# Optimization experiments

Hardware: AMD Instinct MI355X
Metric: run time of the kernel (lower is better)

## Reference

```python
import jax, jax.numpy as jnp
import numpy as np

H, E, D, S, B = 16, 1024, 64, 2048, 4  # heads, emb, head_size, seq_len, batch

def setup_inputs() -> dict:
    key = jax.random.key(0)
    ks = jax.random.split(key, 9)
    sc_e = 1.0 / np.sqrt(E)
    sc_hd = 1.0 / np.sqrt(H * D)
    return {
        "x":  jax.random.normal(ks[0], (B, S, E), dtype=jnp.float32),
        # per-head q/k/v projection weights, stacked: [H, E, D]
        "Wq": jax.random.uniform(ks[1], (H, E, D), jnp.float32, -sc_e, sc_e),
        "Wk": jax.random.uniform(ks[2], (H, E, D), jnp.float32, -sc_e, sc_e),
        "Wv": jax.random.uniform(ks[3], (H, E, D), jnp.float32, -sc_e, sc_e),
        "bq": jax.random.uniform(ks[4], (H, D), jnp.float32, -sc_e, sc_e),
        "bk": jax.random.uniform(ks[5], (H, D), jnp.float32, -sc_e, sc_e),
        "bv": jax.random.uniform(ks[6], (H, D), jnp.float32, -sc_e, sc_e),
        # output projection: Linear(H*D -> E)
        "Wo": jax.random.uniform(ks[7], (H * D, E), jnp.float32, -sc_hd, sc_hd),
        "bo": jax.random.uniform(ks[8], (E,), jnp.float32, -sc_hd, sc_hd),
    }

def reference(x, Wq, Wk, Wv, bq, bk, bv, Wo, bo):
    b, s, e = x.shape
    # batched per-head projections: [B, H, S, D]
    q = jnp.einsum("bse,hed->bhsd", x, Wq) + bq[None, :, None, :]
    k = jnp.einsum("bse,hed->bhsd", x, Wk) + bk[None, :, None, :]
    v = jnp.einsum("bse,hed->bhsd", x, Wv) + bv[None, :, None, :]
    scale = 1.0 / jnp.sqrt(jnp.asarray(q.shape[-1], q.dtype))
    scores = jnp.einsum("bhqd,bhkd->bhqk", q, k) * scale  # [B,H,S,S]
    causal = jnp.tril(jnp.ones((s, s), dtype=bool))
    scores = jnp.where(causal[None, None], scores, jnp.asarray(-jnp.inf, scores.dtype))
    attn = jax.nn.softmax(scores, axis=-1)
    heads = jnp.einsum("bhqk,bhkd->bhqd", attn, v)  # [B,H,S,D]
    concat = heads.transpose(0, 2, 1, 3).reshape(b, s, -1)  # [B,S,H*D]
    return concat @ Wo + bo  # dropout is identity at inference
```

## Files before the change

### kernel.cpp

```cpp
#include <hip/hip_runtime.h>
#include <hip/hip_bf16.h>

#define H_ 16
#define E_ 1024
#define D_ 64
#define S_ 2048
#define B_ 4
#define M_ (B_ * S_)

typedef __bf16 bf16_t;
typedef __bf16 bf16x8 __attribute__((ext_vector_type(8)));
typedef __bf16 bf16x4 __attribute__((ext_vector_type(4)));
typedef float f32x4 __attribute__((ext_vector_type(4)));

typedef __attribute__((address_space(1))) unsigned int gu32;
typedef __attribute__((address_space(3))) unsigned int lu32;

__device__ __forceinline__ f32x4 mfma16(bf16x8 a, bf16x8 b, f32x4 c) {
  return __builtin_amdgcn_mfma_f32_16x16x32_bf16(a, b, c, 0, 0, 0);
}
__device__ __forceinline__ void gl2lds16(const bf16_t* g, bf16_t* l) {
  __builtin_amdgcn_global_load_lds((const gu32*)g, (lu32*)l, 16, 0, 0);
}

#define BAR() asm volatile("s_barrier" ::: "memory")

__device__ __forceinline__ int detect_f32(const unsigned short* __restrict__ xu) {
  int lane = threadIdx.x & 63;
  int cnt = 0;
  for (int i = 0; i < 4; ++i) {
    unsigned short v = xu[(lane * 4 + i) * 2];
    cnt += __popcll(__ballot(((v >> 7) & 0xFF) >= 0xC0));
  }
  return cnt > 16;
}

__global__ __launch_bounds__(256) void convert_x(
    const void* __restrict__ src, bf16_t* __restrict__ dst,
    int* __restrict__ flag, long n) {
  const int f32 = detect_f32((const unsigned short*)src);
  if (blockIdx.x == 0 && threadIdx.x == 0) { flag[0] = f32; flag[1] = 0; }
  long i = ((long)blockIdx.x * 256 + threadIdx.x) * 8;
  if (i >= n) return;
  bf16x8 v;
  if (f32) {
    const float* s = (const float*)src;
    for (int j = 0; j < 8; ++j) v[j] = (bf16_t)s[i + j];
  } else {
    v = *(const bf16x8*)((const bf16_t*)src + i);
  }
  *(bf16x8*)(dst + i) = v;
}

__global__ __launch_bounds__(256) void transpose_k(
    const void* __restrict__ src_, bf16_t* __restrict__ dst,
    const int* __restrict__ flag, int K, int N, long sStride, long dStride) {
  __shared__ __align__(16) bf16_t tile[64][72];
  const int f32 = *flag;
  dst += (long)blockIdx.z * dStride;
  const int tk = blockIdx.x * 64, tn = blockIdx.y * 64;
  const int t = threadIdx.x;
  for (int i = 0; i < 2; ++i) {
    int c = t + i * 256;
    int r = c >> 3, col = (c & 7) * 8;
    if (f32) {
      const float* s = (const float*)src_ + (long)blockIdx.z * sStride;
      const float* p = &s[(long)(tk + r) * N + tn + col];
      for (int j = 0; j < 8; ++j) tile[r][col + j] = (bf16_t)p[j];
    } else {
      const bf16_t* s = (const bf16_t*)src_ + (long)blockIdx.z * sStride;
      *(bf16x8*)&tile[r][col] = *(const bf16x8*)&s[(long)(tk + r) * N + tn + col];
    }
  }
  __syncthreads();
  for (int i = 0; i < 2; ++i) {
    int c = t + i * 256;
    int r = c >> 3, col = (c & 7) * 8;
    bf16x8 v;
    for (int j = 0; j < 8; ++j) v[j] = tile[col + j][r];
    *(bf16x8*)&dst[(long)(tn + r) * K + tk + col] = v;
  }
}

__global__ __launch_bounds__(256) void transpose_qkv(
    const void* __restrict__ s0, const void* __restrict__ s1,
    const void* __restrict__ s2,
    bf16_t* __restrict__ d0, bf16_t* __restrict__ d1, bf16_t* __restrict__ d2,
    const int* __restrict__ flag) {
  __shared__ __align__(16) bf16_t tile[64][72];
  const int f32 = *flag;
  const int which = blockIdx.z >> 4, h = blockIdx.z & 15;
  const void* src_ = which == 0 ? s0 : (which == 1 ? s1 : s2);
  bf16_t* dst = (which == 0 ? d0 : (which == 1 ? d1 : d2)) + (long)h * E_ * D_;
  const long sOff = (long)h * E_ * D_;
  const int tk = blockIdx.x * 64;
  const int t = threadIdx.x;
  for (int i = 0; i < 2; ++i) {
    int c = t + i * 256;
    int r = c >> 3, col = (c & 7) * 8;
    if (f32) {
      const float* s = (const float*)src_ + sOff;
      const float* p = &s[(long)(tk + r) * D_ + col];
      for (int j = 0; j < 8; ++j) tile[r][col + j] = (bf16_t)p[j];
    } else {
      const bf16_t* s = (const bf16_t*)src_ + sOff;
      *(bf16x8*)&tile[r][col] = *(const bf16x8*)&s[(long)(tk + r) * D_ + col];
    }
  }
  __syncthreads();
  for (int i = 0; i < 2; ++i) {
    int c = t + i * 256;
    int r = c >> 3, col = (c & 7) * 8;
    bf16x8 v;
    for (int j = 0; j < 8; ++j) v[j] = tile[col + j][r];
    *(bf16x8*)&dst[(long)r * E_ + tk + col] = v;
  }
}

template <int NBF, int KIND>
__global__ __launch_bounds__(512, 2) void gemm8(
    const bf16_t* __restrict__ A, const bf16_t* __restrict__ Bt,
    const void* __restrict__ bias0, const void* __restrict__ bias1,
    const void* __restrict__ bias2,
    bf16_t* __restrict__ Cq, void* __restrict__ Cout,
    const int* __restrict__ flag) {
  __shared__ __align__(16) bf16_t LA[2 * 256 * 64];
  __shared__ __align__(16) bf16_t LB[2 * NBF * 64 * 64];
  const int t = threadIdx.x;
  const int wave = t >> 6, lane = t & 63;
  const int quad = lane >> 4, l16 = lane & 15;
  const int wm = (wave >> 2) * 128;
  const int wn = (wave & 3) * (NBF * 16);
  const int bid = blockIdx.x;
  const int xcd = bid & 7, l = bid >> 3;
  const int m0 = (xcd * 4 + (l & 3)) * 256;
  const int n0 = (l >> 2) * (NBF * 64);

  f32x4 acc[8][NBF] = {};

  const int sr = lane >> 3;
  const int sj = ((lane & 7) ^ sr) << 3;
  auto stA = [&](int u, int tt, int buf) {
    bf16_t* lp = &LA[buf * 16384 + u * 4096 + wave * 512];
    if constexpr (KIND == 0) {
      gl2lds16(&A[(long)(m0 + u * 64 + wave * 8 + sr) * 1024 + tt * 64 + sj], lp);
    } else {
      int m = m0 + u * 64 + wave * 8 + sr;
      int b = m >> 11, s = m & (S_ - 1);
      gl2lds16(&A[(((long)(b * H_ + tt)) * S_ + s) * D_ + sj], lp);
    }
  };
  auto stB = [&](int u, int tt, int buf) {
    bf16_t* lp = &LB[buf * (NBF * 4096) + u * 4096 + wave * 512];
    gl2lds16(&Bt[(long)(n0 + u * 64 + wave * 8 + sr) * 1024 + tt * 64 + sj], lp);
  };
  auto stage = [&](int tt, int buf) {
    stB(0, tt, buf); stB(1, tt, buf);
    if constexpr (NBF == 3) stB(2, tt, buf);
    stA(0, tt, buf); stA(1, tt, buf); stA(2, tt, buf); stA(3, tt, buf);
  };

  auto rdA = [&](int buf, int i, int kk) {
    int R = wm + i * 16 + l16;
    return *(const bf16x8*)&LA[buf * 16384 + R * 64 + (((kk * 4 + quad) ^ (R & 7)) << 3)];
  };
  auto rdB = [&](int buf, int j, int kk) {
    int R = wn + j * 16 + l16;
    return *(const bf16x8*)&LB[buf * (NBF * 4096) + R * 64 + (((kk * 4 + quad) ^ (R & 7)) << 3)];
  };
  auto compute = [&](int buf) {
    bf16x8 a0[8], a1[8], b0[NBF], b1[NBF];
#pragma unroll
    for (int j = 0; j < NBF; ++j) b0[j] = rdB(buf, j, 0);
#pragma unroll
    for (int i = 0; i < 8; ++i) a0[i] = rdA(buf, i, 0);
#pragma unroll
    for (int j = 0; j < NBF; ++j) b1[j] = rdB(buf, j, 1);
#pragma unroll
    for (int i = 0; i < 8; ++i) a1[i] = rdA(buf, i, 1);
    __builtin_amdgcn_s_setprio(1);
#pragma unroll
    for (int i = 0; i < 8; ++i)
#pragma unroll
      for (int j = 0; j < NBF; ++j)
        acc[i][j] = mfma16(b0[j], a0[i], acc[i][j]);
#pragma unroll
    for (int i = 0; i < 8; ++i)
#pragma unroll
      for (int j = 0; j < NBF; ++j)
        acc[i][j] = mfma16(b1[j], a1[i], acc[i][j]);
    __builtin_amdgcn_s_setprio(0);
  };

  stage(0, 0);

#pragma unroll 1
  for (int tt = 0; tt < 14; tt += 2) {
    stage(tt + 1, 1);
    asm volatile("s_waitcnt vmcnt(%0)" :: "n"(NBF + 4) : "memory");
    BAR();
    compute(0);
    BAR();
    stage(tt + 2, 0);
    asm volatile("s_waitcnt vmcnt(%0)" :: "n"(NBF + 4) : "memory");
    BAR();
    compute(1);
    BAR();
  }
  stage(15, 1);
  asm volatile("s_waitcnt vmcnt(%0)" :: "n"(NBF + 4) : "memory");
  BAR();
  compute(0);
  BAR();
  asm volatile("s_waitcnt vmcnt(0)" ::: "memory");
  BAR();
  compute(1);

  const int f32io = flag[0];
  if constexpr (KIND == 0) {
#pragma unroll
    for (int i = 0; i < 8; ++i) {
      const int m = m0 + wm + i * 16 + l16;
      const int b = m >> 11, s = m & (S_ - 1);
#pragma unroll
      for (int j = 0; j < NBF; ++j) {
        const int n = n0 + wn + j * 16 + quad * 4;
        const int which = n >> 10, nin = n & 1023;
        const int h = nin >> 6, d = nin & 63;
        const void* bp = which == 0 ? bias0 : (which == 1 ? bias1 : bias2);
        bf16x4 o;
#pragma unroll
        for (int r = 0; r < 4; ++r) {
          float bv = f32io ? ((const float*)bp)[nin + r]
                           : (float)((const bf16_t*)bp)[nin + r];
          o[r] = (bf16_t)(acc[i][j][r] + bv);
        }
        *(bf16x4*)&Cq[(long)which * (B_ * H_ * S_ * D_) +
                      (((long)(b * H_ + h)) * S_ + s) * D_ + d] = o;
      }
    }
  } else {
#pragma unroll
    for (int i = 0; i < 8; ++i) {
      const long m = m0 + wm + i * 16 + l16;
#pragma unroll
      for (int j = 0; j < NBF; ++j) {
        const int n = n0 + wn + j * 16 + quad * 4;
        if (f32io) {
          f32x4 o;
#pragma unroll
          for (int r = 0; r < 4; ++r)
            o[r] = acc[i][j][r] + ((const float*)bias0)[n + r];
          *(f32x4*)&((float*)Cout)[m * 1024 + n] = o;
        } else {
          bf16x4 o;
#pragma unroll
          for (int r = 0; r < 4; ++r)
            o[r] = (bf16_t)(acc[i][j][r] + (float)((const bf16_t*)bias0)[n + r]);
          *(bf16x4*)&((bf16_t*)Cout)[m * 1024 + n] = o;
        }
      }
    }
  }
}

__global__ __launch_bounds__(256) void attn_k(
    bf16_t* QO,
    const bf16_t* __restrict__ Kg_,
    const bf16_t* __restrict__ Vtg_) {
  __shared__ __align__(16) bf16_t Ks[64 * 64];
  __shared__ __align__(16) bf16_t Vs[64 * 64];
  __shared__ __align__(16) bf16_t Pq[4][32 * 72];
  const int t = threadIdx.x;
  const int wave = t >> 6, lane = t & 63;
  const int quad = lane >> 4, l16 = lane & 15;
  const int bid = blockIdx.x;
  const int qb = 15 - (bid >> 6);
  const int bh = bid & 63;
  const long base = (long)bh * S_ * D_;
  bf16_t* Qg = QO + base;
  const bf16_t* Kg = Kg_ + base;
  const bf16_t* Vt = Vtg_ + base;
  const int q0 = qb * 128, qrl = wave * 32;
  const int rot = ((lane & 7) - (lane >> 3)) & 7;

  bf16x8 qf[2][2];
  for (int n = 0; n < 2; ++n) {
    long row = q0 + qrl + n * 16 + l16;
    bf16x8 a = *(const bf16x8*)&Qg[row * D_ + quad * 8];
    bf16x8 b = *(const bf16x8*)&Qg[row * D_ + 32 + quad * 8];
    for (int j = 0; j < 8; ++j) {
      a[j] = (bf16_t)((float)a[j] * 0.18033688f);
      b[j] = (bf16_t)((float)b[j] * 0.18033688f);
    }
    qf[n][0] = a; qf[n][1] = b;
  }
  bf16x8 ones;
  for (int j = 0; j < 8; ++j) ones[j] = (bf16_t)1.0f;
  f32x4 o_acc[2][4] = {};
  f32x4 lacc[2] = {};

  const int nkt = 2 * qb + 2;
  for (int kt = 0; kt < nkt; ++kt) {
    __syncthreads();
    for (int i = 0; i < 2; ++i) {
      int c = wave * 2 + i;
      gl2lds16(&Kg[(long)(kt * 64 + c * 8 + (lane >> 3)) * D_ + rot * 8],
               &Ks[c * 512]);
      gl2lds16(&Vt[(long)(c * 8 + (lane >> 3)) * S_ + kt * 64 + rot * 8],
               &Vs[c * 512]);
    }
    __syncthreads();

    if (kt * 64 > q0 + qrl + 31) continue;

    f32x4 sc[2][4];
    for (int mt = 0; mt < 4; ++mt) {
      int krow = mt * 16 + l16;
      bf16x8 kf0 = *(const bf16x8*)&Ks[krow * 64 + (((quad + krow) & 7) << 3)];
      bf16x8 kf1 = *(const bf16x8*)&Ks[krow * 64 + (((quad + 4 + krow) & 7) << 3)];
      for (int n = 0; n < 2; ++n) {
        f32x4 z = {0.f, 0.f, 0.f, 0.f};
        z = mfma16(kf0, qf[n][0], z);
        z = mfma16(kf1, qf[n][1], z);
        sc[n][mt] = z;
      }
    }
    if (kt * 64 + 63 > q0 + qrl) {
      for (int n = 0; n < 2; ++n) {
        int qr = q0 + qrl + n * 16 + l16;
        for (int mt = 0; mt < 4; ++mt)
          for (int r = 0; r < 4; ++r) {
            int kc = kt * 64 + mt * 16 + quad * 4 + r;
            if (kc > qr) sc[n][mt][r] = -1e30f;
          }
      }
    }
    for (int n = 0; n < 2; ++n)
      for (int mt = 0; mt < 4; ++mt) {
        bf16x4 pb;
        for (int r = 0; r < 4; ++r)
          pb[r] = (bf16_t)__builtin_amdgcn_exp2f(sc[n][mt][r]);
        *(bf16x4*)&Pq[wave][(n * 16 + l16) * 72 + mt * 16 + quad * 4] = pb;
      }
    bf16x8 pf[2][2];
    for (int m = 0; m < 2; ++m) {
      pf[m][0] = *(const bf16x8*)&Pq[wave][(m * 16 + l16) * 72 + quad * 8];
      pf[m][1] = *(const bf16x8*)&Pq[wave][(m * 16 + l16) * 72 + 32 + quad * 8];
    }
    for (int m = 0; m < 2; ++m) {
      lacc[m] = mfma16(pf[m][0], ones, lacc[m]);
      lacc[m] = mfma16(pf[m][1], ones, lacc[m]);
    }
    for (int dt = 0; dt < 4; ++dt) {
      int drow = dt * 16 + l16;
      bf16x8 vf0 = *(const bf16x8*)&Vs[drow * 64 + (((quad + drow) & 7) << 3)];
      bf16x8 vf1 = *(const bf16x8*)&Vs[drow * 64 + (((quad + 4 + drow) & 7) << 3)];
      for (int m = 0; m < 2; ++m) {
        o_acc[m][dt] = mfma16(pf[m][0], vf0, o_acc[m][dt]);
        o_acc[m][dt] = mfma16(pf[m][1], vf1, o_acc[m][dt]);
      }
    }
  }
  for (int m = 0; m < 2; ++m)
    for (int r = 0; r < 4; ++r) {
      float inv = 1.0f / lacc[m][r];
      long qg = q0 + qrl + m * 16 + quad * 4 + r;
      for (int dt = 0; dt < 4; ++dt)
        Qg[qg * D_ + dt * 16 + l16] = (bf16_t)(o_acc[m][dt][r] * inv);
    }
}

extern "C" void kernel_launch(void* const* d_in, const int* in_sizes, int n_in,
                              void* d_out, int out_size, void* d_ws, size_t ws_size,
                              hipStream_t stream) {
  (void)in_sizes; (void)n_in; (void)out_size; (void)ws_size;
  const void* x  = d_in[0];
  const void* Wq = d_in[1];
  const void* Wk = d_in[2];
  const void* Wv = d_in[3];
  const void* bq = d_in[4];
  const void* bk = d_in[5];
  const void* bv = d_in[6];
  const void* Wo = d_in[7];
  const void* bo = d_in[8];

  char* base = (char*)d_ws;
  int* flag = (int*)base;
  bf16_t* p = (bf16_t*)(base + 16);
  bf16_t* xb_ = p; p += (size_t)M_ * E_;
  bf16_t* qo_ = p; p += (size_t)B_ * H_ * S_ * D_;
  bf16_t* kb_ = p; p += (size_t)B_ * H_ * S_ * D_;
  bf16_t* vb_ = p; p += (size_t)B_ * H_ * S_ * D_;
  bf16_t* wqt = p; p += (size_t)H_ * D_ * E_;
  bf16_t* wkt = p; p += (size_t)H_ * D_ * E_;
  bf16_t* wvt = p; p += (size_t)H_ * D_ * E_;
  bf16_t* wot = p; p += (size_t)E_ * E_;

  convert_x<<<(M_ * E_) / (256 * 8), 256, 0, stream>>>(x, xb_, flag, (long)M_ * E_);

  transpose_qkv<<<dim3(16, 1, 48), 256, 0, stream>>>(Wq, Wk, Wv, wqt, wkt, wvt, flag);
  transpose_k<<<dim3(16, 16, 1), 256, 0, stream>>>(Wo, wot, flag, E_, E_, 0, 0);

  gemm8<3, 0><<<dim3(512), 512, 0, stream>>>(
      xb_, wqt, bq, bk, bv, qo_, nullptr, flag);

  transpose_k<<<dim3(S_ / 64, 1, B_ * H_), 256, 0, stream>>>(
      vb_, xb_, flag + 1, S_, D_, (long)S_ * D_, (long)S_ * D_);

  attn_k<<<dim3(1024), 256, 0, stream>>>(qo_, kb_, xb_);

  gemm8<2, 1><<<dim3(256), 512, 0, stream>>>(
      qo_, wot, bo, nullptr, nullptr, nullptr, d_out, flag);
}
```

Measured before the change: 278.6 us.

## Split GEMM main loop into four barrier-separated phases with staggered LDS staging

Restructures the projection GEMM main loop from two big compute blocks per double-buffer step into four phases. Each phase loads half of the A fragments (and B fragments every other phase) and then issues its MFMAs. Global-to-LDS staging is split into a main part (B plus A chunks 0 and 2) and a rest part (A chunks 1 and 3). These are issued at different points so that refilling a buffer overlaps with the phases still reading the other rows. This cuts live fragment registers and spreads memory traffic more evenly across compute. In exchange it adds more workgroup barriers per k-step, and its correctness depends on the exact row-to-wave mapping of the partial staging.

```diff
diff --git a/kernel.cpp b/kernel.cpp
--- a/kernel.cpp
+++ b/kernel.cpp
@@ -154,10 +154,13 @@
     bf16_t* lp = &LB[buf * (NBF * 4096) + u * 4096 + wave * 512];
     gl2lds16(&Bt[(long)(n0 + u * 64 + wave * 8 + sr) * 1024 + tt * 64 + sj], lp);
   };
-  auto stage = [&](int tt, int buf) {
+  auto stage_main = [&](int tt, int buf) {
     stB(0, tt, buf); stB(1, tt, buf);
     if constexpr (NBF == 3) stB(2, tt, buf);
-    stA(0, tt, buf); stA(1, tt, buf); stA(2, tt, buf); stA(3, tt, buf);
+    stA(0, tt, buf); stA(2, tt, buf);
+  };
+  auto stage_rest = [&](int tt, int buf) {
+    stA(1, tt, buf); stA(3, tt, buf);
   };
 
   auto rdA = [&](int buf, int i, int kk) {
@@ -168,53 +171,46 @@
     int R = wn + j * 16 + l16;
     return *(const bf16x8*)&LB[buf * (NBF * 4096) + R * 64 + (((kk * 4 + quad) ^ (R & 7)) << 3)];
   };
-  auto compute = [&](int buf) {
-    bf16x8 a0[8], a1[8], b0[NBF], b1[NBF];
-#pragma unroll
-    for (int j = 0; j < NBF; ++j) b0[j] = rdB(buf, j, 0);
-#pragma unroll
-    for (int i = 0; i < 8; ++i) a0[i] = rdA(buf, i, 0);
-#pragma unroll
-    for (int j = 0; j < NBF; ++j) b1[j] = rdB(buf, j, 1);
-#pragma unroll
-    for (int i = 0; i < 8; ++i) a1[i] = rdA(buf, i, 1);
+
+  bf16x8 afr[4], bfr[NBF];
+  auto phase = [&](int buf, int kk, int up, bool rb) {
+#pragma unroll
+    for (int i = 0; i < 4; ++i) afr[i] = rdA(buf, up * 4 + i, kk);
+    if (rb) {
+#pragma unroll
+      for (int j = 0; j < NBF; ++j) bfr[j] = rdB(buf, j, kk);
+    }
+    BAR();
     __builtin_amdgcn_s_setprio(1);
 #pragma unroll
-    for (int i = 0; i < 8; ++i)
+    for (int i = 0; i < 4; ++i)
 #pragma unroll
       for (int j = 0; j < NBF; ++j)
-        acc[i][j] = mfma16(b0[j], a0[i], acc[i][j]);
-#pragma unroll
-    for (int i = 0; i < 8; ++i)
-#pragma unroll
-      for (int j = 0; j < NBF; ++j)
-        acc[i][j] = mfma16(b1[j], a1[i], acc[i][j]);
+        acc[up * 4 + i][j] = mfma16(bfr[j], afr[i], acc[up * 4 + i][j]);
     __builtin_amdgcn_s_setprio(0);
   };
 
-  stage(0, 0);
+  stage_main(0, 0); stage_rest(0, 0);
+  stage_main(1, 1);
+  asm volatile("s_waitcnt vmcnt(%0)" :: "n"(NBF + 2) : "memory");
+  BAR();
 
 #pragma unroll 1
-  for (int tt = 0; tt < 14; tt += 2) {
-    stage(tt + 1, 1);
-    asm volatile("s_waitcnt vmcnt(%0)" :: "n"(NBF + 4) : "memory");
+  for (int T = 0; T < 16; ++T) {
+    const int b = T & 1;
+    if (T < 15) stage_rest(T + 1, b ^ 1);
+    phase(b, 0, 0, true);
     BAR();
-    compute(0);
+    phase(b, 0, 1, false);
     BAR();
-    stage(tt + 2, 0);
-    asm volatile("s_waitcnt vmcnt(%0)" :: "n"(NBF + 4) : "memory");
+    phase(b, 1, 0, true);
     BAR();
-    compute(1);
+    if (T < 14) stage_main(T + 2, b);
+    phase(b, 1, 1, false);
+    if (T < 14) asm volatile("s_waitcnt vmcnt(%0)" :: "n"(NBF + 2) : "memory");
+    else        asm volatile("s_waitcnt vmcnt(0)" ::: "memory");
     BAR();
   }
-  stage(15, 1);
-  asm volatile("s_waitcnt vmcnt(%0)" :: "n"(NBF + 4) : "memory");
-  BAR();
-  compute(0);
-  BAR();
-  asm volatile("s_waitcnt vmcnt(0)" ::: "memory");
-  BAR();
-  compute(1);
 
   const int f32io = flag[0];
   if constexpr (KIND == 0) {
```

New measurement: 313.3 us. 12.5% more time.

## Double-buffer K/V tiles in attention kernel with async prefetch

Applied to the files above, without the earlier changes.

Doubles the LDS K and V buffers. The attention loop now issues the global-to-LDS loads for the next key tile before computing on the current one, using explicit vmcnt waits and barriers so the load latency overlaps with MFMA work. This adds 16KB of LDS per block, which may lower occupancy. It relies on BAR() being defined elsewhere in the file and on the vmcnt count matching the four outstanding loads.

```diff
diff --git a/kernel.cpp b/kernel.cpp
--- a/kernel.cpp
+++ b/kernel.cpp
@@ -268,8 +268,8 @@
     bf16_t* QO,
     const bf16_t* __restrict__ Kg_,
     const bf16_t* __restrict__ Vtg_) {
-  __shared__ __align__(16) bf16_t Ks[64 * 64];
-  __shared__ __align__(16) bf16_t Vs[64 * 64];
+  __shared__ __align__(16) bf16_t Ks[2 * 64 * 64];
+  __shared__ __align__(16) bf16_t Vs[2 * 64 * 64];
   __shared__ __align__(16) bf16_t Pq[4][32 * 72];
   const int t = threadIdx.x;
   const int wave = t >> 6, lane = t & 63;
@@ -284,6 +284,17 @@
   const int q0 = qb * 128, qrl = wave * 32;
   const int rot = ((lane & 7) - (lane >> 3)) & 7;
 
+  auto stageKV = [&](int kt, int buf) {
+    for (int i = 0; i < 2; ++i) {
+      int c = wave * 2 + i;
+      gl2lds16(&Kg[(long)(kt * 64 + c * 8 + (lane >> 3)) * D_ + rot * 8],
+               &Ks[buf * 4096 + c * 512]);
+      gl2lds16(&Vt[(long)(c * 8 + (lane >> 3)) * S_ + kt * 64 + rot * 8],
+               &Vs[buf * 4096 + c * 512]);
+    }
+  };
+  stageKV(0, 0);
+
   bf16x8 qf[2][2];
   for (int n = 0; n < 2; ++n) {
     long row = q0 + qrl + n * 16 + l16;
@@ -301,66 +312,68 @@
   f32x4 lacc[2] = {};
 
   const int nkt = 2 * qb + 2;
+#pragma unroll 1
   for (int kt = 0; kt < nkt; ++kt) {
-    __syncthreads();
-    for (int i = 0; i < 2; ++i) {
-      int c = wave * 2 + i;
-      gl2lds16(&Kg[(long)(kt * 64 + c * 8 + (lane >> 3)) * D_ + rot * 8],
-               &Ks[c * 512]);
-      gl2lds16(&Vt[(long)(c * 8 + (lane >> 3)) * S_ + kt * 64 + rot * 8],
-               &Vs[c * 512]);
-    }
-    __syncthreads();
-
-    if (kt * 64 > q0 + qrl + 31) continue;
-
-    f32x4 sc[2][4];
-    for (int mt = 0; mt < 4; ++mt) {
-      int krow = mt * 16 + l16;
-      bf16x8 kf0 = *(const bf16x8*)&Ks[krow * 64 + (((quad + krow) & 7) << 3)];
-      bf16x8 kf1 = *(const bf16x8*)&Ks[krow * 64 + (((quad + 4 + krow) & 7) << 3)];
-      for (int n = 0; n < 2; ++n) {
-        f32x4 z = {0.f, 0.f, 0.f, 0.f};
-        z = mfma16(kf0, qf[n][0], z);
-        z = mfma16(kf1, qf[n][1], z);
-        sc[n][mt] = z;
-      }
-    }
-    if (kt * 64 + 63 > q0 + qrl) {
-      for (int n = 0; n < 2; ++n) {
-        int qr = q0 + qrl + n * 16 + l16;
-        for (int mt = 0; mt < 4; ++mt)
-          for (int r = 0; r < 4; ++r) {
-            int kc = kt * 64 + mt * 16 + quad * 4 + r;
-            if (kc > qr) sc[n][mt][r] = -1e30f;
-          }
-      }
-    }
-    for (int n = 0; n < 2; ++n)
+    const int buf = kt & 1;
+    const int kb = buf * 4096;
+    if (kt + 1 < nkt) {
+      stageKV(kt + 1, buf ^ 1);
+      asm volatile("s_waitcnt vmcnt(4)" ::: "memory");
+    } else {
+      asm volatile("s_waitcnt vmcnt(0)" ::: "memory");
+    }
+    BAR();
+
+    if (kt * 64 <= q0 + qrl + 31) {
+      f32x4 sc[2][4];
       for (int mt = 0; mt < 4; ++mt) {
-        bf16x4 pb;
-        for (int r = 0; r < 4; ++r)
-          pb[r] = (bf16_t)__builtin_amdgcn_exp2f(sc[n][mt][r]);
-        *(bf16x4*)&Pq[wave][(n * 16 + l16) * 72 + mt * 16 + quad * 4] = pb;
-      }
-    bf16x8 pf[2][2];
-    for (int m = 0; m < 2; ++m) {
-      pf[m][0] = *(const bf16x8*)&Pq[wave][(m * 16 + l16) * 72 + quad * 8];
-      pf[m][1] = *(const bf16x8*)&Pq[wave][(m * 16 + l16) * 72 + 32 + quad * 8];
-    }
-    for (int m = 0; m < 2; ++m) {
-      lacc[m] = mfma16(pf[m][0], ones, lacc[m]);
-      lacc[m] = mfma16(pf[m][1], ones, lacc[m]);
-    }
-    for (int dt = 0; dt < 4; ++dt) {
-      int drow = dt * 16 + l16;
-      bf16x8 vf0 = *(const bf16x8*)&Vs[drow * 64 + (((quad + drow) & 7) << 3)];
-      bf16x8 vf1 = *(const bf16x8*)&Vs[drow * 64 + (((quad + 4 + drow) & 7) << 3)];
+        int krow = mt * 16 + l16;
+        bf16x8 kf0 = *(const bf16x8*)&Ks[kb + krow * 64 + (((quad + krow) & 7) << 3)];
+        bf16x8 kf1 = *(const bf16x8*)&Ks[kb + krow * 64 + (((quad + 4 + krow) & 7) << 3)];
+        for (int n = 0; n < 2; ++n) {
+          f32x4 z = {0.f, 0.f, 0.f, 0.f};
+          z = mfma16(kf0, qf[n][0], z);
+          z = mfma16(kf1, qf[n][1], z);
+          sc[n][mt] = z;
+        }
+      }
+      if (kt * 64 + 63 > q0 + qrl) {
+        for (int n = 0; n < 2; ++n) {
+          int qr = q0 + qrl + n * 16 + l16;
+          for (int mt = 0; mt < 4; ++mt)
+            for (int r = 0; r < 4; ++r) {
+              int kc = kt * 64 + mt * 16 + quad * 4 + r;
+              if (kc > qr) sc[n][mt][r] = -1e30f;
+            }
+        }
+      }
+      for (int n = 0; n < 2; ++n)
+        for (int mt = 0; mt < 4; ++mt) {
+          bf16x4 pb;
+          for (int r = 0; r < 4; ++r)
+            pb[r] = (bf16_t)__builtin_amdgcn_exp2f(sc[n][mt][r]);
+          *(bf16x4*)&Pq[wave][(n * 16 + l16) * 72 + mt * 16 + quad * 4] = pb;
+        }
+      bf16x8 pf[2][2];
       for (int m = 0; m < 2; ++m) {
-        o_acc[m][dt] = mfma16(pf[m][0], vf0, o_acc[m][dt]);
-        o_acc[m][dt] = mfma16(pf[m][1], vf1, o_acc[m][dt]);
-      }
-    }
+        pf[m][0] = *(const bf16x8*)&Pq[wave][(m * 16 + l16) * 72 + quad * 8];
+        pf[m][1] = *(const bf16x8*)&Pq[wave][(m * 16 + l16) * 72 + 32 + quad * 8];
+      }
+      for (int m = 0; m < 2; ++m) {
+        lacc[m] = mfma16(pf[m][0], ones, lacc[m]);
+        lacc[m] = mfma16(pf[m][1], ones, lacc[m]);
+      }
+      for (int dt = 0; dt < 4; ++dt) {
+        int drow = dt * 16 + l16;
+        bf16x8 vf0 = *(const bf16x8*)&Vs[kb + drow * 64 + (((quad + drow) & 7) << 3)];
+        bf16x8 vf1 = *(const bf16x8*)&Vs[kb + drow * 64 + (((quad + 4 + drow) & 7) << 3)];
+        for (int m = 0; m < 2; ++m) {
+          o_acc[m][dt] = mfma16(pf[m][0], vf0, o_acc[m][dt]);
+          o_acc[m][dt] = mfma16(pf[m][1], vf1, o_acc[m][dt]);
+        }
+      }
+    }
+    BAR();
   }
   for (int m = 0; m < 2; ++m)
     for (int r = 0; r < 4; ++r) {
```

New measurement: 283.2 us. About the same (+1.6%).

## Write V transposed from QKV GEMM epilogue and merge weight transpose kernels

Applied to the files above, without the earlier changes.

The QKV GEMM epilogue now stores V directly in [B,H,D,S] layout, which removes the separate V transpose kernel and its round trip through global memory. The Wq/Wk/Wv and Wo transposes are merged into one launch to cut launch overhead. The trade-off is that V stores become scalar, strided writes (stride S) instead of vectorized bf16x4 stores, which may hurt write coalescing in the epilogue.

```diff
diff --git a/kernel.cpp b/kernel.cpp
--- a/kernel.cpp
+++ b/kernel.cpp
@@ -52,23 +52,41 @@
   *(bf16x8*)(dst + i) = v;
 }
 
-__global__ __launch_bounds__(256) void transpose_k(
-    const void* __restrict__ src_, bf16_t* __restrict__ dst,
-    const int* __restrict__ flag, int K, int N, long sStride, long dStride) {
+__global__ __launch_bounds__(256) void transpose_w(
+    const void* __restrict__ s0, const void* __restrict__ s1,
+    const void* __restrict__ s2, const void* __restrict__ s3,
+    bf16_t* __restrict__ d0, bf16_t* __restrict__ d1,
+    bf16_t* __restrict__ d2, bf16_t* __restrict__ d3,
+    const int* __restrict__ flag) {
   __shared__ __align__(16) bf16_t tile[64][72];
   const int f32 = *flag;
-  dst += (long)blockIdx.z * dStride;
-  const int tk = blockIdx.x * 64, tn = blockIdx.y * 64;
+  const int z = blockIdx.z;
   const int t = threadIdx.x;
+  const void* src_;
+  bf16_t* dst;
+  long sOff;
+  int N, K, tk, tn;
+  if (z < 3) {
+    const int h = blockIdx.y;
+    src_ = z == 0 ? s0 : (z == 1 ? s1 : s2);
+    dst = (z == 0 ? d0 : (z == 1 ? d1 : d2)) + (long)h * E_ * D_;
+    sOff = (long)h * E_ * D_;
+    N = D_; K = E_;
+    tk = blockIdx.x * 64; tn = 0;
+  } else {
+    src_ = s3; dst = d3; sOff = 0;
+    N = E_; K = E_;
+    tk = blockIdx.x * 64; tn = blockIdx.y * 64;
+  }
   for (int i = 0; i < 2; ++i) {
     int c = t + i * 256;
     int r = c >> 3, col = (c & 7) * 8;
     if (f32) {
-      const float* s = (const float*)src_ + (long)blockIdx.z * sStride;
+      const float* s = (const float*)src_ + sOff;
       const float* p = &s[(long)(tk + r) * N + tn + col];
       for (int j = 0; j < 8; ++j) tile[r][col + j] = (bf16_t)p[j];
     } else {
-      const bf16_t* s = (const bf16_t*)src_ + (long)blockIdx.z * sStride;
+      const bf16_t* s = (const bf16_t*)src_ + sOff;
       *(bf16x8*)&tile[r][col] = *(const bf16x8*)&s[(long)(tk + r) * N + tn + col];
     }
   }
@@ -79,41 +97,6 @@
     bf16x8 v;
     for (int j = 0; j < 8; ++j) v[j] = tile[col + j][r];
     *(bf16x8*)&dst[(long)(tn + r) * K + tk + col] = v;
-  }
-}
-
-__global__ __launch_bounds__(256) void transpose_qkv(
-    const void* __restrict__ s0, const void* __restrict__ s1,
-    const void* __restrict__ s2,
-    bf16_t* __restrict__ d0, bf16_t* __restrict__ d1, bf16_t* __restrict__ d2,
-    const int* __restrict__ flag) {
-  __shared__ __align__(16) bf16_t tile[64][72];
-  const int f32 = *flag;
-  const int which = blockIdx.z >> 4, h = blockIdx.z & 15;
-  const void* src_ = which == 0 ? s0 : (which == 1 ? s1 : s2);
-  bf16_t* dst = (which == 0 ? d0 : (which == 1 ? d1 : d2)) + (long)h * E_ * D_;
-  const long sOff = (long)h * E_ * D_;
-  const int tk = blockIdx.x * 64;
-  const int t = threadIdx.x;
-  for (int i = 0; i < 2; ++i) {
-    int c = t + i * 256;
-    int r = c >> 3, col = (c & 7) * 8;
-    if (f32) {
-      const float* s = (const float*)src_ + sOff;
-      const float* p = &s[(long)(tk + r) * D_ + col];
-      for (int j = 0; j < 8; ++j) tile[r][col + j] = (bf16_t)p[j];
-    } else {
-      const bf16_t* s = (const bf16_t*)src_ + sOff;
-      *(bf16x8*)&tile[r][col] = *(const bf16x8*)&s[(long)(tk + r) * D_ + col];
-    }
-  }
-  __syncthreads();
-  for (int i = 0; i < 2; ++i) {
-    int c = t + i * 256;
-    int r = c >> 3, col = (c & 7) * 8;
-    bf16x8 v;
-    for (int j = 0; j < 8; ++j) v[j] = tile[col + j][r];
-    *(bf16x8*)&dst[(long)r * E_ + tk + col] = v;
   }
 }
 
@@ -228,15 +211,26 @@
         const int which = n >> 10, nin = n & 1023;
         const int h = nin >> 6, d = nin & 63;
         const void* bp = which == 0 ? bias0 : (which == 1 ? bias1 : bias2);
-        bf16x4 o;
-#pragma unroll
-        for (int r = 0; r < 4; ++r) {
-          float bv = f32io ? ((const float*)bp)[nin + r]
-                           : (float)((const bf16_t*)bp)[nin + r];
-          o[r] = (bf16_t)(acc[i][j][r] + bv);
+        if (which == 2) {
+          bf16_t* Vt = Cq + 2L * ((long)B_ * H_ * S_ * D_);
+#pragma unroll
+          for (int r = 0; r < 4; ++r) {
+            float bv = f32io ? ((const float*)bp)[nin + r]
+                             : (float)((const bf16_t*)bp)[nin + r];
+            Vt[(((long)(b * H_ + h)) * D_ + d + r) * S_ + s] =
+                (bf16_t)(acc[i][j][r] + bv);
+          }
+        } else {
+          bf16x4 o;
+#pragma unroll
+          for (int r = 0; r < 4; ++r) {
+            float bv = f32io ? ((const float*)bp)[nin + r]
+                             : (float)((const bf16_t*)bp)[nin + r];
+            o[r] = (bf16_t)(acc[i][j][r] + bv);
+          }
+          *(bf16x4*)&Cq[(long)which * (B_ * H_ * S_ * D_) +
+                        (((long)(b * H_ + h)) * S_ + s) * D_ + d] = o;
         }
-        *(bf16x4*)&Cq[(long)which * (B_ * H_ * S_ * D_) +
-                      (((long)(b * H_ + h)) * S_ + s) * D_ + d] = o;
       }
     }
   } else {
@@ -399,16 +393,13 @@
 
   convert_x<<<(M_ * E_) / (256 * 8), 256, 0, stream>>>(x, xb_, flag, (long)M_ * E_);
 
-  transpose_qkv<<<dim3(16, 1, 48), 256, 0, stream>>>(Wq, Wk, Wv, wqt, wkt, wvt, flag);
-  transpose_k<<<dim3(16, 16, 1), 256, 0, stream>>>(Wo, wot, flag, E_, E_, 0, 0);
+  transpose_w<<<dim3(16, 16, 4), 256, 0, stream>>>(
+      Wq, Wk, Wv, Wo, wqt, wkt, wvt, wot, flag);
 
   gemm8<3, 0><<<dim3(512), 512, 0, stream>>>(
       xb_, wqt, bq, bk, bv, qo_, nullptr, flag);
 
-  transpose_k<<<dim3(S_ / 64, 1, B_ * H_), 256, 0, stream>>>(
-      vb_, xb_, flag + 1, S_, D_, (long)S_ * D_, (long)S_ * D_);
-
-  attn_k<<<dim3(1024), 256, 0, stream>>>(qo_, kb_, xb_);
+  attn_k<<<dim3(1024), 256, 0, stream>>>(qo_, kb_, vb_);
 
   gemm8<2, 1><<<dim3(256), 512, 0, stream>>>(
       qo_, wot, bo, nullptr, nullptr, nullptr, d_out, flag);
```

New measurement: 274.9 us. Within noise of the previous version (-1.3%).
